# Kernel optimization log

Measured on AMD Instinct MI355X. Metric: run time of the kernel, lower is better.

## Reference

```python
import jax, jax.numpy as jnp
import numpy as np

B = 16384      # batch
IN = 151       # input dim (layer_widths[0])
HID = 200      # RBF out_features (layer_widths[1])
CENT = 2000    # layer_centres[0]


def setup_inputs() -> dict:
    key = jax.random.key(0)
    ks = jax.random.split(key, 6)
    x = jax.random.normal(ks[0], (B, IN), dtype=jnp.float32)
    # RBF params per reset_parameters: centres ~ N(0, 0.01), sigmas = 2
    centres = 0.01 * jax.random.normal(ks[1], (HID, IN), dtype=jnp.float32)
    sigmas = jnp.full((HID,), 2.0, dtype=jnp.float32)
    # Linear layers (torch layout: weight is (out, in))
    w1 = jax.random.normal(ks[2], (CENT, HID), dtype=jnp.float32) / jnp.sqrt(jnp.float32(HID))
    b1 = jnp.zeros((CENT,), dtype=jnp.float32)
    # small scale so exp() stays well-conditioned
    w2 = 0.001 * jax.random.normal(ks[3], (CENT, CENT), dtype=jnp.float32)
    b2 = jnp.zeros((CENT,), dtype=jnp.float32)
    # kernel matrix (151, 2000); positive so Ehat[:, 0] > 0
    kern = jax.random.uniform(ks[4], (IN, CENT), dtype=jnp.float32)
    return {"x": x, "centres": centres, "sigmas": sigmas,
            "w1": w1, "b1": b1, "w2": w2, "b2": b2, "kern": kern}


def reference(x, centres, sigmas, w1, b1, w2, b2, kern):
    # RBF layer: distances_ij = ||x_i - c_j||_2 * sigma_j ; phi = exp(-distances^2)
    # exp(-(sqrt(d2)*sigma)^2) == exp(-d2 * sigma^2), so we skip the sqrt and the
    # (B, CENT, IN) expand tensor entirely.
    x2 = jnp.sum(x * x, axis=1, keepdims=True)            # (B, 1)
    c2 = jnp.sum(centres * centres, axis=1)[None, :]      # (1, HID)
    d2 = jnp.maximum(x2 + c2 - 2.0 * (x @ centres.T), 0.0)  # (B, HID)
    phi = jnp.exp(-d2 * (sigmas * sigmas)[None, :])       # (B, HID)

    h = jax.nn.relu(phi @ w1.T + b1)                      # (B, CENT)
    out = jnp.exp(h @ w2.T + b2)                          # (B, CENT)

    Ehat = out @ kern.T                                   # (B, IN)  == matmul(kern, out.T).T
    Rhat = out / Ehat[:, :1]                              # divide by correction term Ehat[:, 0]
    Ehat2 = Rhat @ kern.T                                 # (B, IN)
    return (Ehat2, Rhat, Ehat2, Rhat, x)
```

## Files before the change

### kernel.cpp

```cpp
#include <hip/hip_runtime.h>

#define BDIM 16384
#define IN_D 151
#define HID_D 200
#define CENT_D 2000

#define INP 192
#define HIDP 256
#define CENTP 2048
#define KERN_R 192

using bf16x8 = __attribute__((ext_vector_type(8))) short;
using f32x4  = __attribute__((ext_vector_type(4))) float;
using f4     = __attribute__((ext_vector_type(4))) float;
using us4    = __attribute__((ext_vector_type(4))) unsigned short;
using us8    = __attribute__((ext_vector_type(8))) unsigned short;
using i32x4  = __attribute__((ext_vector_type(4))) int;
using i32x8  = __attribute__((ext_vector_type(8))) int;

__device__ __forceinline__ unsigned short f2bf(float f) {
  unsigned u = __builtin_bit_cast(unsigned, f);
  u += 0x7FFFu + ((u >> 16) & 1u);
  return (unsigned short)(u >> 16);
}
__device__ __forceinline__ float bf2f(unsigned short h) {
  unsigned u = ((unsigned)h) << 16;
  return __builtin_bit_cast(float, u);
}
__device__ __forceinline__ unsigned char f2fp8(float f) {
  return (unsigned char)(__builtin_amdgcn_cvt_pk_fp8_f32(f, f, 0, false) & 0xFF);
}

typedef __attribute__((address_space(1))) const unsigned int guint;
typedef __attribute__((address_space(3))) unsigned int luint;
__device__ __forceinline__ void g2l16(const void* g, void* l) {
  __builtin_amdgcn_global_load_lds((guint*)g, (luint*)l, 16, 0, 0);
}

struct G0Args {
  const unsigned short* A;
  const unsigned short* B;
  const float* x2; const float* c2; const float* sg2;
  unsigned char* o8;
};

__global__ __launch_bounds__(256) void gemm_phi(G0Args p) {
  __shared__ __align__(16) short As[128 * 64];
  __shared__ __align__(16) short Bs[128 * 64];
  const int tid  = threadIdx.x;
  const int lane = tid & 63;
  const int w    = tid >> 6;
  const int wr   = w >> 1, wc = w & 1;
  const int lr   = lane & 15;
  const int tm = blockIdx.x, tn = blockIdx.y;
  f32x4 acc[4][4] = {};

  const unsigned short* Ag = p.A + (size_t)tm * 128 * INP;
  const unsigned short* Bg = p.B + (size_t)tn * 128 * INP;

  int rowc[4], colc[4], ldsc[4];
#pragma unroll
  for (int i = 0; i < 4; i++) {
    int cc = i * 256 + tid;
    rowc[i] = cc >> 3;
    colc[i] = ((cc & 7) ^ (rowc[i] & 7)) * 8;
    ldsc[i] = cc * 8;
  }

  for (int k0 = 0; k0 < INP; k0 += 64) {
    __syncthreads();
#pragma unroll
    for (int i = 0; i < 4; i++)
      g2l16(Ag + (size_t)rowc[i] * INP + k0 + colc[i], &As[ldsc[i]]);
#pragma unroll
    for (int i = 0; i < 4; i++)
      g2l16(Bg + (size_t)rowc[i] * INP + k0 + colc[i], &Bs[ldsc[i]]);
    __syncthreads();
#pragma unroll
    for (int ks = 0; ks < 2; ks++) {
      bf16x8 af[4], bfr[4];
#pragma unroll
      for (int m = 0; m < 4; m++) {
        int r = wr * 64 + m * 16 + lr;
        af[m] = *(const bf16x8*)&As[r * 64 + ((((ks << 2) + (lane >> 4)) ^ (r & 7)) << 3)];
      }
#pragma unroll
      for (int n = 0; n < 4; n++) {
        int r = wc * 64 + n * 16 + lr;
        bfr[n] = *(const bf16x8*)&Bs[r * 64 + ((((ks << 2) + (lane >> 4)) ^ (r & 7)) << 3)];
      }
#pragma unroll
      for (int m = 0; m < 4; m++)
#pragma unroll
        for (int n = 0; n < 4; n++)
          acc[m][n] = __builtin_amdgcn_mfma_f32_16x16x32_bf16(af[m], bfr[n], acc[m][n], 0, 0, 0);
    }
  }

  const int rb = tm * 128 + wr * 64 + (lane >> 4) * 4;
  const int cb = tn * 128 + wc * 64 + lr;
#pragma unroll
  for (int m = 0; m < 4; m++) {
#pragma unroll
    for (int n = 0; n < 4; n++) {
      const int gj = cb + n * 16;
#pragma unroll
      for (int r = 0; r < 4; r++) {
        const int gi = rb + m * 16 + r;
        float ph = 0.f;
        if (gj < HID_D) {
          float d2 = fmaxf(p.x2[gi] + p.c2[gj] - 2.f * acc[m][n][r], 0.f);
          ph = __expf(-d2 * p.sg2[gj]);
        }
        p.o8[(size_t)gi * HIDP + gj] = f2fp8(ph);
      }
    }
  }
}

struct G8Args {
  const unsigned char* A;
  const unsigned char* B;
  int K;
  const float* bias;
  unsigned short* obf;
  unsigned char* o8;
};

template<int MODE>
__global__ __launch_bounds__(256) void gemm_fp8(G8Args p) {
  __shared__ __align__(16) unsigned char As[128 * 128];
  __shared__ __align__(16) unsigned char Bs[128 * 128];
  const int tid  = threadIdx.x;
  const int lane = tid & 63;
  const int w    = tid >> 6;
  const int wr   = w >> 1, wc = w & 1;
  const int lr   = lane & 15;
  const int g    = lane >> 4;
  const int tm = blockIdx.x, tn = blockIdx.y;
  const int K = p.K;
  f32x4 acc[4][4] = {};

  const unsigned char* Ag = p.A + (size_t)tm * 128 * K;
  const unsigned char* Bg = p.B + (size_t)tn * 128 * K;

  int rowc[4], colb[4], ldsb[4];
#pragma unroll
  for (int i = 0; i < 4; i++) {
    int cc = i * 256 + tid;
    rowc[i] = cc >> 3;
    colb[i] = ((cc & 7) ^ (rowc[i] & 7)) << 4;
    ldsb[i] = cc << 4;
  }

  for (int k0 = 0; k0 < K; k0 += 128) {
    __syncthreads();
#pragma unroll
    for (int i = 0; i < 4; i++)
      g2l16(Ag + (size_t)rowc[i] * K + k0 + colb[i], &As[ldsb[i]]);
#pragma unroll
    for (int i = 0; i < 4; i++)
      g2l16(Bg + (size_t)rowc[i] * K + k0 + colb[i], &Bs[ldsb[i]]);
    __syncthreads();

    i32x8 bfr[4];
#pragma unroll
    for (int n = 0; n < 4; n++) {
      const int r = wc * 64 + n * 16 + lr;
      const int rb_ = r << 7, rx = r & 7;
      i32x4 lo = *(const i32x4*)&Bs[rb_ + (((2 * g) ^ rx) << 4)];
      i32x4 hi = *(const i32x4*)&Bs[rb_ + (((2 * g + 1) ^ rx) << 4)];
      bfr[n][0] = lo[0]; bfr[n][1] = lo[1]; bfr[n][2] = lo[2]; bfr[n][3] = lo[3];
      bfr[n][4] = hi[0]; bfr[n][5] = hi[1]; bfr[n][6] = hi[2]; bfr[n][7] = hi[3];
    }
#pragma unroll
    for (int m = 0; m < 4; m++) {
      const int r = wr * 64 + m * 16 + lr;
      const int rb_ = r << 7, rx = r & 7;
      i32x4 lo = *(const i32x4*)&As[rb_ + (((2 * g) ^ rx) << 4)];
      i32x4 hi = *(const i32x4*)&As[rb_ + (((2 * g + 1) ^ rx) << 4)];
      i32x8 av;
      av[0] = lo[0]; av[1] = lo[1]; av[2] = lo[2]; av[3] = lo[3];
      av[4] = hi[0]; av[5] = hi[1]; av[6] = hi[2]; av[7] = hi[3];
#pragma unroll
      for (int n = 0; n < 4; n++)
        acc[m][n] = __builtin_amdgcn_mfma_scale_f32_16x16x128_f8f6f4(
            av, bfr[n], acc[m][n], 0, 0, 0, 127, 0, 127);
    }
  }

  const int rb = tm * 128 + wr * 64 + (lane >> 4) * 4;
  const int cb = tn * 128 + wc * 64 + lr;
  const float rs = (MODE == 1) ? 0.125f : (1.0f / 256.0f);
#pragma unroll
  for (int m = 0; m < 4; m++) {
#pragma unroll
    for (int n = 0; n < 4; n++) {
      const int gj = cb + n * 16;
      const float b = (gj < CENT_D) ? p.bias[gj] : 0.f;
#pragma unroll
      for (int r = 0; r < 4; r++) {
        const int gi = rb + m * 16 + r;
        if constexpr (MODE == 1) {
          p.o8[(size_t)gi * CENTP + gj] = f2fp8(fmaxf(acc[m][n][r] * rs + b, 0.f));
        } else {
          float o = (gj < CENT_D) ? __expf(acc[m][n][r] * rs + b) : 0.f;
          p.obf[(size_t)gi * CENTP + gj] = f2bf(o);
        }
      }
    }
  }
}

struct G3Args {
  const unsigned short* A;
  const unsigned short* B;
  float* of;
  int kspan;
};

__global__ __launch_bounds__(256, 1) void gemm3w(G3Args p) {
  __shared__ __align__(16) short As[128 * 64];
  __shared__ __align__(16) short Bs[KERN_R * 64];
  const int tid  = threadIdx.x;
  const int lane = tid & 63;
  const int w    = tid >> 6;
  const int wr   = w >> 1, wc = w & 1;
  const int lr   = lane & 15;
  const int tm = blockIdx.x;
  const int kbeg = blockIdx.y * p.kspan;
  f32x4 acc[4][6] = {};

  const unsigned short* Ag = p.A + (size_t)tm * 128 * CENTP;
  const unsigned short* Bg = p.B;

  int rowa[4], cola[4], lda_[4];
#pragma unroll
  for (int i = 0; i < 4; i++) {
    int cc = i * 256 + tid;
    rowa[i] = cc >> 3;
    cola[i] = ((cc & 7) ^ (rowa[i] & 7)) * 8;
    lda_[i] = cc * 8;
  }
  int rowb[6], colbb[6], ldb_[6];
#pragma unroll
  for (int i = 0; i < 6; i++) {
    int cc = i * 256 + tid;
    rowb[i] = cc >> 3;
    colbb[i] = ((cc & 7) ^ (rowb[i] & 7)) * 8;
    ldb_[i] = cc * 8;
  }

  for (int k0 = kbeg; k0 < kbeg + p.kspan; k0 += 64) {
    __syncthreads();
#pragma unroll
    for (int i = 0; i < 4; i++)
      g2l16(Ag + (size_t)rowa[i] * CENTP + k0 + cola[i], &As[lda_[i]]);
#pragma unroll
    for (int i = 0; i < 6; i++)
      g2l16(Bg + (size_t)rowb[i] * CENTP + k0 + colbb[i], &Bs[ldb_[i]]);
    __syncthreads();
#pragma unroll
    for (int ks = 0; ks < 2; ks++) {
      bf16x8 af[4], bfr[6];
#pragma unroll
      for (int m = 0; m < 4; m++) {
        int r = wr * 64 + m * 16 + lr;
        af[m] = *(const bf16x8*)&As[r * 64 + ((((ks << 2) + (lane >> 4)) ^ (r & 7)) << 3)];
      }
#pragma unroll
      for (int n = 0; n < 6; n++) {
        int r = wc * 96 + n * 16 + lr;
        bfr[n] = *(const bf16x8*)&Bs[r * 64 + ((((ks << 2) + (lane >> 4)) ^ (r & 7)) << 3)];
      }
#pragma unroll
      for (int m = 0; m < 4; m++)
#pragma unroll
        for (int n = 0; n < 6; n++)
          acc[m][n] = __builtin_amdgcn_mfma_f32_16x16x32_bf16(af[m], bfr[n], acc[m][n], 0, 0, 0);
    }
  }

  float* of = p.of + (size_t)blockIdx.y * BDIM * IN_D;
  const int rb = tm * 128 + wr * 64 + (lane >> 4) * 4;
  const int cb = wc * 96 + lr;
#pragma unroll
  for (int m = 0; m < 4; m++) {
#pragma unroll
    for (int n = 0; n < 6; n++) {
      const int gj = cb + n * 16;
#pragma unroll
      for (int r = 0; r < 4; r++) {
        const int gi = rb + m * 16 + r;
        if (gj < IN_D) of[(size_t)gi * IN_D + gj] = acc[m][n][r];
      }
    }
  }
}

__global__ __launch_bounds__(256) void prep_cast(
    const float* __restrict__ x, const float* __restrict__ cen,
    const float* __restrict__ kern,
    unsigned short* __restrict__ x_bf, unsigned short* __restrict__ c_bf,
    unsigned short* __restrict__ kernp) {
  const int c = blockIdx.x * 256 + threadIdx.x;
  const float* src; unsigned short* dst; int R, C, cpq, local, vec;
  if (c < 786432)       { src = x;    dst = x_bf;  R = 16384; C = 151;  cpq = 48;  local = c;           vec = 0; }
  else if (c < 798720)  { src = cen;  dst = c_bf;  R = 200;   C = 151;  cpq = 48;  local = c - 786432;  vec = 0; }
  else                  { src = kern; dst = kernp; R = 151;   C = 2000; cpq = 512; local = c - 798720;  vec = 1; }
  const int r  = local / cpq;
  const int c4 = (local - r * cpq) << 2;
  us4 o;
  if (vec && r < R && c4 + 3 < C) {
    f4 v = *(const f4*)&src[(size_t)r * C + c4];
    o[0] = f2bf(v[0]); o[1] = f2bf(v[1]); o[2] = f2bf(v[2]); o[3] = f2bf(v[3]);
  } else {
#pragma unroll
    for (int k = 0; k < 4; k++) {
      float v = (r < R && c4 + k < C) ? src[(size_t)r * C + c4 + k] : 0.f;
      o[k] = f2bf(v);
    }
  }
  *(us4*)&dst[(size_t)local * 4] = o;
}

__global__ __launch_bounds__(256) void prep_lowp(
    const float* __restrict__ w1, const float* __restrict__ w2,
    unsigned char* __restrict__ w1p8, unsigned char* __restrict__ w2p8) {
  const int i = blockIdx.x * 256 + threadIdx.x;
  const float* src; unsigned char* dst; int r, c4, R, C; float sc;
  int j;
  if (i < 131072) { src = w1; dst = w1p8; j = i;          r = j >> 6; c4 = (j & 63) << 2;  R = 2000; C = 200;  sc = 8.f; }
  else            { src = w2; dst = w2p8; j = i - 131072; r = j >> 9; c4 = (j & 511) << 2; R = 2000; C = 2000; sc = 256.f; }
  float v[4];
#pragma unroll
  for (int k = 0; k < 4; k++)
    v[k] = (r < R && c4 + k < C) ? src[(size_t)r * C + c4 + k] * sc : 0.f;
  int p0 = __builtin_amdgcn_cvt_pk_fp8_f32(v[0], v[1], 0, false);
  int p1 = __builtin_amdgcn_cvt_pk_fp8_f32(v[2], v[3], 0, false);
  *(unsigned int*)&dst[(size_t)j * 4] =
      ((unsigned)p0 & 0xFFFFu) | (((unsigned)p1 & 0xFFFFu) << 16);
}

__global__ __launch_bounds__(256) void prep_misc(
    const float* __restrict__ x, const float* __restrict__ cen,
    const float* __restrict__ sg,
    float* __restrict__ x2, float* __restrict__ c2, float* __restrict__ sg2) {
  const int b = blockIdx.x;
  if (b == 4160) {
    int j = threadIdx.x;
    sg2[j] = (j < HID_D) ? sg[j] * sg[j] : 0.f;
    return;
  }
  const float* src; float* dst; int R, base;
  if (b < 4096) { src = x;   dst = x2; R = BDIM;  base = b * 4; }
  else          { src = cen; dst = c2; R = HID_D; base = (b - 4096) * 4; }
  const int row = base + (threadIdx.x >> 6);
  const int l = threadIdx.x & 63;
  float s = 0.f;
  if (row < R)
    for (int k = l; k < IN_D; k += 64) { float v = src[(size_t)row * IN_D + k]; s += v * v; }
#pragma unroll
  for (int off = 32; off > 0; off >>= 1) s += __shfl_down(s, off);
  if (l == 0) dst[row] = s;
}

__global__ __launch_bounds__(256) void finalize(
    float* __restrict__ dout, const unsigned short* __restrict__ outp,
    const float* __restrict__ x, const float* __restrict__ part) {
  const int i = blockIdx.x;
  const size_t SL = (size_t)BDIM * IN_D;
  float* Eh = dout;
  float* Ra = dout + SL;
  float* Eb = dout + SL + (size_t)BDIM * CENT_D;
  float* Rb = Eb + SL;
  float* xo = Rb + (size_t)BDIM * CENT_D;
  const size_t ib = (size_t)i * IN_D;
  const float e0 = part[ib] + part[SL + ib] + part[2 * SL + ib] + part[3 * SL + ib];
  const float s = 1.f / e0;
  const int t = threadIdx.x;
  if (t < IN_D) {
    float v = (part[ib + t] + part[SL + ib + t] + part[2 * SL + ib + t] + part[3 * SL + ib + t]) * s;
    Eh[ib + t] = v;
    Eb[ib + t] = v;
    xo[ib + t] = x[ib + t];
  }
  if (t < 250) {
    const us8 u = *(const us8*)&outp[(size_t)i * CENTP + t * 8];
    f4 a, b;
#pragma unroll
    for (int k = 0; k < 4; k++) a[k] = bf2f(u[k]) * s;
#pragma unroll
    for (int k = 0; k < 4; k++) b[k] = bf2f(u[4 + k]) * s;
    const size_t o = (size_t)i * CENT_D + t * 8;
    *(f4*)&Ra[o] = a; *(f4*)&Ra[o + 4] = b;
    *(f4*)&Rb[o] = a; *(f4*)&Rb[o + 4] = b;
  }
}

extern "C" void kernel_launch(void* const* d_in, const int* in_sizes, int n_in,
                              void* d_out, int out_size, void* d_ws, size_t ws_size,
                              hipStream_t stream) {
  (void)in_sizes; (void)n_in; (void)out_size; (void)ws_size;
  const float* x       = (const float*)d_in[0];
  const float* centres = (const float*)d_in[1];
  const float* sigmas  = (const float*)d_in[2];
  const float* w1      = (const float*)d_in[3];
  const float* b1      = (const float*)d_in[4];
  const float* w2      = (const float*)d_in[5];
  const float* b2      = (const float*)d_in[6];
  const float* kern    = (const float*)d_in[7];
  float* dout = (float*)d_out;

  char* ws = (char*)d_ws;
  size_t off = 0;
  auto alloc = [&](size_t bytes) {
    char* p = ws + off;
    off = (off + bytes + 255) & ~(size_t)255;
    return p;
  };
  unsigned short* x_bf  = (unsigned short*)alloc((size_t)BDIM * INP * 2);
  unsigned short* c_bf  = (unsigned short*)alloc((size_t)256 * INP * 2);
  unsigned char*  w1p8  = (unsigned char*)alloc((size_t)CENTP * HIDP);
  unsigned char*  w2p8  = (unsigned char*)alloc((size_t)CENTP * CENTP);
  unsigned short* kernp = (unsigned short*)alloc((size_t)KERN_R * CENTP * 2);
  unsigned char*  phip8 = (unsigned char*)alloc((size_t)BDIM * HIDP);
  unsigned short* outp  = (unsigned short*)alloc((size_t)BDIM * CENTP * 2);
  float* x2  = (float*)alloc((size_t)BDIM * 4);
  float* c2  = (float*)alloc((size_t)256 * 4);
  float* sg2 = (float*)alloc((size_t)256 * 4);
  float* eparts = (float*)alloc((size_t)4 * BDIM * IN_D * 4);
  unsigned char* hp8 = (unsigned char*)(dout + (size_t)BDIM * (2 * IN_D + CENT_D));

  prep_cast<<<3504, 256, 0, stream>>>(x, centres, kern, x_bf, c_bf, kernp);
  prep_lowp<<<4608, 256, 0, stream>>>(w1, w2, w1p8, w2p8);
  prep_misc<<<4161, 256, 0, stream>>>(x, centres, sigmas, x2, c2, sg2);

  G0Args g0{}; g0.A = x_bf; g0.B = c_bf;
  g0.x2 = x2; g0.c2 = c2; g0.sg2 = sg2; g0.o8 = phip8;
  gemm_phi<<<dim3(BDIM / 128, HIDP / 128), 256, 0, stream>>>(g0);

  G8Args g1{}; g1.A = phip8; g1.B = w1p8; g1.K = HIDP;
  g1.bias = b1; g1.o8 = hp8;
  gemm_fp8<1><<<dim3(BDIM / 128, CENTP / 128), 256, 0, stream>>>(g1);

  G8Args g2{}; g2.A = hp8; g2.B = w2p8; g2.K = CENTP;
  g2.bias = b2; g2.obf = outp;
  gemm_fp8<2><<<dim3(BDIM / 128, CENTP / 128), 256, 0, stream>>>(g2);

  G3Args g3{}; g3.A = outp; g3.B = kernp; g3.of = eparts; g3.kspan = CENTP / 4;
  gemm3w<<<dim3(BDIM / 128, 4), 256, 0, stream>>>(g3);

  finalize<<<BDIM, 256, 0, stream>>>(dout, outp, x, eparts);
}
```

Before: 244.3 us.

## Merge prep kernels, halve phi GEMM tile, reduce final GEMM split-K to two

Folds the three preprocessing kernels into a single launch and moves the copy of x to the output into the cast pass, taking it out of finalize. Shrinks the phi GEMM M-tile from 128 to 64 rows so more blocks are launched. Cuts the split-K factor of the kern GEMM from four to two, which halves the partial-sum traffic finalize has to read. In exchange each gemm3w block does a longer K loop, with half as many blocks in flight.

```diff
diff --git a/kernel.cpp b/kernel.cpp
--- a/kernel.cpp
+++ b/kernel.cpp
@@ -45,7 +45,7 @@
 };
 
 __global__ __launch_bounds__(256) void gemm_phi(G0Args p) {
-  __shared__ __align__(16) short As[128 * 64];
+  __shared__ __align__(16) short As[64 * 64];
   __shared__ __align__(16) short Bs[128 * 64];
   const int tid  = threadIdx.x;
   const int lane = tid & 63;
@@ -53,35 +53,43 @@
   const int wr   = w >> 1, wc = w & 1;
   const int lr   = lane & 15;
   const int tm = blockIdx.x, tn = blockIdx.y;
-  f32x4 acc[4][4] = {};
-
-  const unsigned short* Ag = p.A + (size_t)tm * 128 * INP;
+  f32x4 acc[2][4] = {};
+
+  const unsigned short* Ag = p.A + (size_t)tm * 64 * INP;
   const unsigned short* Bg = p.B + (size_t)tn * 128 * INP;
 
-  int rowc[4], colc[4], ldsc[4];
+  int rowa[2], cola[2], lda_[2];
+#pragma unroll
+  for (int i = 0; i < 2; i++) {
+    int cc = i * 256 + tid;
+    rowa[i] = cc >> 3;
+    cola[i] = ((cc & 7) ^ (rowa[i] & 7)) * 8;
+    lda_[i] = cc * 8;
+  }
+  int rowb[4], colb[4], ldb_[4];
 #pragma unroll
   for (int i = 0; i < 4; i++) {
     int cc = i * 256 + tid;
-    rowc[i] = cc >> 3;
-    colc[i] = ((cc & 7) ^ (rowc[i] & 7)) * 8;
-    ldsc[i] = cc * 8;
+    rowb[i] = cc >> 3;
+    colb[i] = ((cc & 7) ^ (rowb[i] & 7)) * 8;
+    ldb_[i] = cc * 8;
   }
 
   for (int k0 = 0; k0 < INP; k0 += 64) {
     __syncthreads();
 #pragma unroll
+    for (int i = 0; i < 2; i++)
+      g2l16(Ag + (size_t)rowa[i] * INP + k0 + cola[i], &As[lda_[i]]);
+#pragma unroll
     for (int i = 0; i < 4; i++)
-      g2l16(Ag + (size_t)rowc[i] * INP + k0 + colc[i], &As[ldsc[i]]);
-#pragma unroll
-    for (int i = 0; i < 4; i++)
-      g2l16(Bg + (size_t)rowc[i] * INP + k0 + colc[i], &Bs[ldsc[i]]);
+      g2l16(Bg + (size_t)rowb[i] * INP + k0 + colb[i], &Bs[ldb_[i]]);
     __syncthreads();
 #pragma unroll
     for (int ks = 0; ks < 2; ks++) {
-      bf16x8 af[4], bfr[4];
-#pragma unroll
-      for (int m = 0; m < 4; m++) {
-        int r = wr * 64 + m * 16 + lr;
+      bf16x8 af[2], bfr[4];
+#pragma unroll
+      for (int m = 0; m < 2; m++) {
+        int r = wr * 32 + m * 16 + lr;
         af[m] = *(const bf16x8*)&As[r * 64 + ((((ks << 2) + (lane >> 4)) ^ (r & 7)) << 3)];
       }
 #pragma unroll
@@ -90,17 +98,17 @@
         bfr[n] = *(const bf16x8*)&Bs[r * 64 + ((((ks << 2) + (lane >> 4)) ^ (r & 7)) << 3)];
       }
 #pragma unroll
-      for (int m = 0; m < 4; m++)
+      for (int m = 0; m < 2; m++)
 #pragma unroll
         for (int n = 0; n < 4; n++)
           acc[m][n] = __builtin_amdgcn_mfma_f32_16x16x32_bf16(af[m], bfr[n], acc[m][n], 0, 0, 0);
     }
   }
 
-  const int rb = tm * 128 + wr * 64 + (lane >> 4) * 4;
+  const int rb = tm * 64 + wr * 32 + (lane >> 4) * 4;
   const int cb = tn * 128 + wc * 64 + lr;
 #pragma unroll
-  for (int m = 0; m < 4; m++) {
+  for (int m = 0; m < 2; m++) {
 #pragma unroll
     for (int n = 0; n < 4; n++) {
       const int gj = cb + n * 16;
@@ -298,92 +306,93 @@
   }
 }
 
-__global__ __launch_bounds__(256) void prep_cast(
+#define NB_CAST 3504
+#define NB_LOWP 4608
+#define NB_MISC 4161
+
+__global__ __launch_bounds__(256) void prep_all(
     const float* __restrict__ x, const float* __restrict__ cen,
-    const float* __restrict__ kern,
+    const float* __restrict__ kern, const float* __restrict__ w1,
+    const float* __restrict__ w2, const float* __restrict__ sg,
     unsigned short* __restrict__ x_bf, unsigned short* __restrict__ c_bf,
-    unsigned short* __restrict__ kernp) {
-  const int c = blockIdx.x * 256 + threadIdx.x;
-  const float* src; unsigned short* dst; int R, C, cpq, local, vec;
-  if (c < 786432)       { src = x;    dst = x_bf;  R = 16384; C = 151;  cpq = 48;  local = c;           vec = 0; }
-  else if (c < 798720)  { src = cen;  dst = c_bf;  R = 200;   C = 151;  cpq = 48;  local = c - 786432;  vec = 0; }
-  else                  { src = kern; dst = kernp; R = 151;   C = 2000; cpq = 512; local = c - 798720;  vec = 1; }
-  const int r  = local / cpq;
-  const int c4 = (local - r * cpq) << 2;
-  us4 o;
-  if (vec && r < R && c4 + 3 < C) {
-    f4 v = *(const f4*)&src[(size_t)r * C + c4];
-    o[0] = f2bf(v[0]); o[1] = f2bf(v[1]); o[2] = f2bf(v[2]); o[3] = f2bf(v[3]);
+    unsigned short* __restrict__ kernp, unsigned char* __restrict__ w1p8,
+    unsigned char* __restrict__ w2p8, float* __restrict__ x2,
+    float* __restrict__ c2, float* __restrict__ sg2,
+    float* __restrict__ xo) {
+  const int b = blockIdx.x;
+  if (b < NB_CAST) {
+    const int c = b * 256 + threadIdx.x;
+    const float* src; unsigned short* dst; int R, C, cpq, local, vec, isx;
+    if (c < 786432)      { src = x;    dst = x_bf;  R = 16384; C = 151;  cpq = 48;  local = c;           vec = 0; isx = 1; }
+    else if (c < 798720) { src = cen;  dst = c_bf;  R = 200;   C = 151;  cpq = 48;  local = c - 786432;  vec = 0; isx = 0; }
+    else                 { src = kern; dst = kernp; R = 151;   C = 2000; cpq = 512; local = c - 798720;  vec = 1; isx = 0; }
+    const int r  = local / cpq;
+    const int c4 = (local - r * cpq) << 2;
+    us4 o;
+    if (vec && r < R && c4 + 3 < C) {
+      f4 v = *(const f4*)&src[(size_t)r * C + c4];
+      o[0] = f2bf(v[0]); o[1] = f2bf(v[1]); o[2] = f2bf(v[2]); o[3] = f2bf(v[3]);
+    } else {
+#pragma unroll
+      for (int k = 0; k < 4; k++) {
+        float v = (r < R && c4 + k < C) ? src[(size_t)r * C + c4 + k] : 0.f;
+        o[k] = f2bf(v);
+        if (isx && c4 + k < C) xo[(size_t)r * IN_D + c4 + k] = v;
+      }
+    }
+    *(us4*)&dst[(size_t)local * 4] = o;
+  } else if (b < NB_CAST + NB_LOWP) {
+    const int i = (b - NB_CAST) * 256 + threadIdx.x;
+    const float* src; unsigned char* dst; int r, c4, R, C; float sc;
+    int j;
+    if (i < 131072) { src = w1; dst = w1p8; j = i;          r = j >> 6; c4 = (j & 63) << 2;  R = 2000; C = 200;  sc = 8.f; }
+    else            { src = w2; dst = w2p8; j = i - 131072; r = j >> 9; c4 = (j & 511) << 2; R = 2000; C = 2000; sc = 256.f; }
+    float v[4];
+#pragma unroll
+    for (int k = 0; k < 4; k++)
+      v[k] = (r < R && c4 + k < C) ? src[(size_t)r * C + c4 + k] * sc : 0.f;
+    int p0 = __builtin_amdgcn_cvt_pk_fp8_f32(v[0], v[1], 0, false);
+    int p1 = __builtin_amdgcn_cvt_pk_fp8_f32(v[2], v[3], 0, false);
+    *(unsigned int*)&dst[(size_t)j * 4] =
+        ((unsigned)p0 & 0xFFFFu) | (((unsigned)p1 & 0xFFFFu) << 16);
   } else {
-#pragma unroll
-    for (int k = 0; k < 4; k++) {
-      float v = (r < R && c4 + k < C) ? src[(size_t)r * C + c4 + k] : 0.f;
-      o[k] = f2bf(v);
-    }
-  }
-  *(us4*)&dst[(size_t)local * 4] = o;
-}
-
-__global__ __launch_bounds__(256) void prep_lowp(
-    const float* __restrict__ w1, const float* __restrict__ w2,
-    unsigned char* __restrict__ w1p8, unsigned char* __restrict__ w2p8) {
-  const int i = blockIdx.x * 256 + threadIdx.x;
-  const float* src; unsigned char* dst; int r, c4, R, C; float sc;
-  int j;
-  if (i < 131072) { src = w1; dst = w1p8; j = i;          r = j >> 6; c4 = (j & 63) << 2;  R = 2000; C = 200;  sc = 8.f; }
-  else            { src = w2; dst = w2p8; j = i - 131072; r = j >> 9; c4 = (j & 511) << 2; R = 2000; C = 2000; sc = 256.f; }
-  float v[4];
-#pragma unroll
-  for (int k = 0; k < 4; k++)
-    v[k] = (r < R && c4 + k < C) ? src[(size_t)r * C + c4 + k] * sc : 0.f;
-  int p0 = __builtin_amdgcn_cvt_pk_fp8_f32(v[0], v[1], 0, false);
-  int p1 = __builtin_amdgcn_cvt_pk_fp8_f32(v[2], v[3], 0, false);
-  *(unsigned int*)&dst[(size_t)j * 4] =
-      ((unsigned)p0 & 0xFFFFu) | (((unsigned)p1 & 0xFFFFu) << 16);
-}
-
-__global__ __launch_bounds__(256) void prep_misc(
-    const float* __restrict__ x, const float* __restrict__ cen,
-    const float* __restrict__ sg,
-    float* __restrict__ x2, float* __restrict__ c2, float* __restrict__ sg2) {
-  const int b = blockIdx.x;
-  if (b == 4160) {
-    int j = threadIdx.x;
-    sg2[j] = (j < HID_D) ? sg[j] * sg[j] : 0.f;
-    return;
-  }
-  const float* src; float* dst; int R, base;
-  if (b < 4096) { src = x;   dst = x2; R = BDIM;  base = b * 4; }
-  else          { src = cen; dst = c2; R = HID_D; base = (b - 4096) * 4; }
-  const int row = base + (threadIdx.x >> 6);
-  const int l = threadIdx.x & 63;
-  float s = 0.f;
-  if (row < R)
-    for (int k = l; k < IN_D; k += 64) { float v = src[(size_t)row * IN_D + k]; s += v * v; }
-#pragma unroll
-  for (int off = 32; off > 0; off >>= 1) s += __shfl_down(s, off);
-  if (l == 0) dst[row] = s;
+    const int b2 = b - NB_CAST - NB_LOWP;
+    if (b2 == 4160) {
+      int j = threadIdx.x;
+      sg2[j] = (j < HID_D) ? sg[j] * sg[j] : 0.f;
+      return;
+    }
+    const float* src; float* dst; int R, base;
+    if (b2 < 4096) { src = x;   dst = x2; R = BDIM;  base = b2 * 4; }
+    else           { src = cen; dst = c2; R = HID_D; base = (b2 - 4096) * 4; }
+    const int row = base + (threadIdx.x >> 6);
+    const int l = threadIdx.x & 63;
+    float s = 0.f;
+    if (row < R)
+      for (int k = l; k < IN_D; k += 64) { float v = src[(size_t)row * IN_D + k]; s += v * v; }
+#pragma unroll
+    for (int off = 32; off > 0; off >>= 1) s += __shfl_down(s, off);
+    if (l == 0) dst[row] = s;
+  }
 }
 
 __global__ __launch_bounds__(256) void finalize(
     float* __restrict__ dout, const unsigned short* __restrict__ outp,
-    const float* __restrict__ x, const float* __restrict__ part) {
+    const float* __restrict__ part) {
   const int i = blockIdx.x;
   const size_t SL = (size_t)BDIM * IN_D;
   float* Eh = dout;
   float* Ra = dout + SL;
   float* Eb = dout + SL + (size_t)BDIM * CENT_D;
   float* Rb = Eb + SL;
-  float* xo = Rb + (size_t)BDIM * CENT_D;
   const size_t ib = (size_t)i * IN_D;
-  const float e0 = part[ib] + part[SL + ib] + part[2 * SL + ib] + part[3 * SL + ib];
+  const float e0 = part[ib] + part[SL + ib];
   const float s = 1.f / e0;
   const int t = threadIdx.x;
   if (t < IN_D) {
-    float v = (part[ib + t] + part[SL + ib + t] + part[2 * SL + ib + t] + part[3 * SL + ib + t]) * s;
+    float v = (part[ib + t] + part[SL + ib + t]) * s;
     Eh[ib + t] = v;
     Eb[ib + t] = v;
-    xo[ib + t] = x[ib + t];
   }
   if (t < 250) {
     const us8 u = *(const us8*)&outp[(size_t)i * CENTP + t * 8];
@@ -429,16 +438,17 @@
   float* x2  = (float*)alloc((size_t)BDIM * 4);
   float* c2  = (float*)alloc((size_t)256 * 4);
   float* sg2 = (float*)alloc((size_t)256 * 4);
-  float* eparts = (float*)alloc((size_t)4 * BDIM * IN_D * 4);
+  float* eparts = (float*)alloc((size_t)2 * BDIM * IN_D * 4);
   unsigned char* hp8 = (unsigned char*)(dout + (size_t)BDIM * (2 * IN_D + CENT_D));
-
-  prep_cast<<<3504, 256, 0, stream>>>(x, centres, kern, x_bf, c_bf, kernp);
-  prep_lowp<<<4608, 256, 0, stream>>>(w1, w2, w1p8, w2p8);
-  prep_misc<<<4161, 256, 0, stream>>>(x, centres, sigmas, x2, c2, sg2);
+  float* xo = dout + (size_t)BDIM * (2 * IN_D + 2 * CENT_D);
+
+  prep_all<<<NB_CAST + NB_LOWP + NB_MISC, 256, 0, stream>>>(
+      x, centres, kern, w1, w2, sigmas,
+      x_bf, c_bf, kernp, w1p8, w2p8, x2, c2, sg2, xo);
 
   G0Args g0{}; g0.A = x_bf; g0.B = c_bf;
   g0.x2 = x2; g0.c2 = c2; g0.sg2 = sg2; g0.o8 = phip8;
-  gemm_phi<<<dim3(BDIM / 128, HIDP / 128), 256, 0, stream>>>(g0);
+  gemm_phi<<<dim3(BDIM / 64, HIDP / 128), 256, 0, stream>>>(g0);
 
   G8Args g1{}; g1.A = phip8; g1.B = w1p8; g1.K = HIDP;
   g1.bias = b1; g1.o8 = hp8;
@@ -448,8 +458,8 @@
   g2.bias = b2; g2.obf = outp;
   gemm_fp8<2><<<dim3(BDIM / 128, CENTP / 128), 256, 0, stream>>>(g2);
 
-  G3Args g3{}; g3.A = outp; g3.B = kernp; g3.of = eparts; g3.kspan = CENTP / 4;
-  gemm3w<<<dim3(BDIM / 128, 4), 256, 0, stream>>>(g3);
-
-  finalize<<<BDIM, 256, 0, stream>>>(dout, outp, x, eparts);
-}
+  G3Args g3{}; g3.A = outp; g3.B = kernp; g3.of = eparts; g3.kspan = CENTP / 2;
+  gemm3w<<<dim3(BDIM / 128, 2), 256, 0, stream>>>(g3);
+
+  finalize<<<BDIM, 256, 0, stream>>>(dout, outp, eparts);
+}
```

After: 232.6 us. -4.8%, faster.
